# Performance work log

Measured on AMD Instinct MI355X. Metric: run time of the kernel, lower is better.

Reference implementation:

```python
import jax, jax.numpy as jnp
import numpy as np

HEADS = 4
RATES = (1, 2, 3, 4)
BN_EPS = 1e-5


def setup_inputs() -> dict:
    key = jax.random.key(0)
    k1, k2, k3 = jax.random.split(key, 3)
    b, c, h, w = 4, 256, 128, 128
    x = jax.random.normal(k1, (b, c, h, w), dtype=jnp.float32)
    w_qkv = jax.random.normal(k2, (3 * c, c), dtype=jnp.float32) * 0.02
    w_proj = jax.random.normal(k3, (c, c), dtype=jnp.float32) * 0.02
    gamma = jnp.ones((c,), dtype=jnp.float32)
    beta = jnp.zeros((c,), dtype=jnp.float32)
    return {"x": x, "w_qkv": w_qkv, "w_proj": w_proj, "gamma": gamma, "beta": beta}


def _neighbors(t, r, h, w):
    # t: [b, d, h, w] -> [b, d, 9, h, w], 3x3 dilated window with zero padding
    # (row-major kernel-position order matches F.unfold's C x kh x kw layout).
    tp = jnp.pad(t, ((0, 0), (0, 0), (r, r), (r, r)))
    return jnp.stack(
        [tp[:, :, i * r:i * r + h, j * r:j * r + w] for i in range(3) for j in range(3)],
        axis=2,
    )


def reference(x, w_qkv, w_proj, gamma, beta):
    b, c, h, w = x.shape
    d = c // HEADS
    # 1x1 conv == channel matmul
    qkv = jnp.einsum('oc,bchw->bohw', w_qkv, x)
    q, k, v = jnp.split(qkv, 3, axis=1)
    q = q.reshape(b, HEADS, d, h, w)
    k = k.reshape(b, HEADS, d, h, w)
    v = v.reshape(b, HEADS, d, h, w)
    outs = []
    for hi, r in enumerate(RATES):
        qh = q[:, hi]                      # [b, d, h, w]
        k_n = _neighbors(k[:, hi], r, h, w)  # [b, d, 9, h, w]
        v_n = _neighbors(v[:, hi], r, h, w)  # [b, d, 9, h, w]
        scores = jnp.einsum('bdhw,bdnhw->bnhw', qh, k_n)  # [b, 9, h, w]
        attn = jax.nn.softmax(scores, axis=1)
        outs.append(jnp.einsum('bdnhw,bnhw->bdhw', v_n, attn))
    y = jnp.concatenate(outs, axis=1)      # [b, c, h, w]
    y = jnp.einsum('oc,bchw->bohw', w_proj, y)
    # BatchNorm2d (training-mode batch statistics, biased variance)
    mean = y.mean(axis=(0, 2, 3), keepdims=True)
    var = ((y - mean) ** 2).mean(axis=(0, 2, 3), keepdims=True)
    yn = (y - mean) * jax.lax.rsqrt(var + BN_EPS)
    yn = yn * gamma[None, :, None, None] + beta[None, :, None, None]
    return x + jax.nn.silu(yn)
```

## Files before the change

### kernel.cpp

```cpp
#include <hip/hip_runtime.h>
#include <hip/hip_bf16.h>

#define BATCH 4
#define CCH   256
#define HH    128
#define WW    128
#define HWSZ  (HH * WW)
#define NHEADS 4
#define DHEAD 64
#define KDIM  256
#define PDIM  16384

typedef unsigned short u16;
typedef short bf16x8 __attribute__((ext_vector_type(8)));
typedef float f32x4  __attribute__((ext_vector_type(4)));

__device__ __forceinline__ float bf2f(u16 u) {
    return __uint_as_float(((unsigned)u) << 16);
}
__device__ __forceinline__ u16 f2bf(float f) {
    unsigned u = __float_as_uint(f);
    unsigned r = (u + 0x7fffu + ((u >> 16) & 1u)) >> 16;
    return (u16)r;
}
__device__ __forceinline__ unsigned pack2(float a, float b) {
    return (unsigned)f2bf(a) | ((unsigned)f2bf(b) << 16);
}
__device__ __forceinline__ void gl_lds16(const u16* g, u16* l) {
    __builtin_amdgcn_global_load_lds(
        (const __attribute__((address_space(1))) void*)g,
        (__attribute__((address_space(3))) void*)l, 16, 0, 0);
}

__global__ __launch_bounds__(256) void wconv(
    const float* __restrict__ wq, const float* __restrict__ wp,
    u16* __restrict__ wqb, u16* __restrict__ wpb)
{
    const int i = (blockIdx.x * 256 + threadIdx.x) * 4;
    const float4 v = (i < 196608)
        ? *reinterpret_cast<const float4*>(&wq[i])
        : *reinterpret_cast<const float4*>(&wp[i - 196608]);
    ushort4 o;
    o.x = f2bf(v.x); o.y = f2bf(v.y); o.z = f2bf(v.z); o.w = f2bf(v.w);
    if (i < 196608) *reinterpret_cast<ushort4*>(&wqb[i]) = o;
    else            *reinterpret_cast<ushort4*>(&wpb[i - 196608]) = o;
}

__global__ __launch_bounds__(256) void transpose_x(
    const float* __restrict__ x, u16* __restrict__ XT)
{
    __shared__ float t[32][33];
    const int b  = blockIdx.z;
    const int c0 = blockIdx.y * 32;
    const int p0 = blockIdx.x * 32;
    const int tid = threadIdx.x;

    #pragma unroll
    for (int it = 0; it < 4; ++it) {
        const int r = it * 8 + (tid >> 5);
        const int col = tid & 31;
        t[r][col] = x[((size_t)b * CCH + c0 + r) * HWSZ + p0 + col];
    }
    __syncthreads();
    #pragma unroll
    for (int it = 0; it < 2; ++it) {
        const int prow = it * 16 + (tid >> 4);
        const int cpair = (tid & 15) * 2;
        const float v0 = t[cpair][prow];
        const float v1 = t[cpair + 1][prow];
        ushort2 o; o.x = f2bf(v0); o.y = f2bf(v1);
        *reinterpret_cast<ushort2*>(
            &XT[((size_t)b * HWSZ + p0 + prow) * CCH + c0 + cpair]) = o;
    }
}

template <int OUT_MODE>
__global__ __launch_bounds__(256) void gemm_mfma(
    const u16* __restrict__ A, const u16* __restrict__ B,
    void* __restrict__ Y, long long b_zs,
    float* __restrict__ part, int batch0)
{
    constexpr int BK = 64;
    __shared__ u16 As[128 * BK];
    __shared__ u16 Bs[128 * BK];

    const int tid  = threadIdx.x;
    const int lane = tid & 63;
    const int w    = tid >> 6;
    const int wm   = w >> 1, wn = w & 1;
    const int o0   = blockIdx.y * 128;
    const int p0   = blockIdx.x * 128;
    const u16* Bz  = B + (size_t)blockIdx.z * b_zs;

    const int srow  = lane >> 3;
    const int sslot = (lane & 7) ^ srow;

    auto stage = [&](int c0) {
        #pragma unroll
        for (int j = 0; j < 4; ++j) {
            const int q = w * 4 + j;
            const int r = q * 8 + srow;
            gl_lds16(A  + (size_t)(o0 + r) * KDIM + c0 + sslot * 8, As + q * 512);
            gl_lds16(Bz + (size_t)(p0 + r) * KDIM + c0 + sslot * 8, Bs + q * 512);
        }
    };

    f32x4 acc[4][4];
    #pragma unroll
    for (int m = 0; m < 4; ++m)
        #pragma unroll
        for (int n = 0; n < 4; ++n)
            acc[m][n] = (f32x4){0.f, 0.f, 0.f, 0.f};

    stage(0);
    #pragma unroll
    for (int kt = 0; kt < KDIM / BK; ++kt) {
        __syncthreads();
        #pragma unroll
        for (int h = 0; h < 2; ++h) {
            bf16x8 af[4], bfr[4];
            #pragma unroll
            for (int m = 0; m < 4; ++m) {
                const int r  = wm * 64 + m * 16 + (lane & 15);
                const int sl = ((h << 2) | (lane >> 4)) ^ (r & 7);
                af[m] = *reinterpret_cast<const bf16x8*>(As + r * BK + sl * 8);
            }
            #pragma unroll
            for (int n = 0; n < 4; ++n) {
                const int r  = wn * 64 + n * 16 + (lane & 15);
                const int sl = ((h << 2) | (lane >> 4)) ^ (r & 7);
                bfr[n] = *reinterpret_cast<const bf16x8*>(Bs + r * BK + sl * 8);
            }
            #pragma unroll
            for (int m = 0; m < 4; ++m)
                #pragma unroll
                for (int n = 0; n < 4; ++n)
                    acc[m][n] = __builtin_amdgcn_mfma_f32_16x16x32_bf16(
                        af[m], bfr[n], acc[m][n], 0, 0, 0);
        }
        if (kt + 1 < KDIM / BK) {
            __syncthreads();
            stage((kt + 1) * BK);
        }
    }

    const int g = lane >> 4, ln15 = lane & 15;
    if (OUT_MODE == 1) {
        const int batch = batch0 + blockIdx.z;
        u16* Yz = (u16*)Y + (size_t)batch * CCH * HWSZ;
        float s[4][4], q2[4][4];
        #pragma unroll
        for (int m = 0; m < 4; ++m) {
            const int ow = o0 + wm * 64 + m * 16 + g * 4;
            #pragma unroll
            for (int j = 0; j < 4; ++j) { s[m][j] = 0.f; q2[m][j] = 0.f; }
            #pragma unroll
            for (int n = 0; n < 4; ++n) {
                const int pc = p0 + wn * 64 + n * 16 + ln15;
                #pragma unroll
                for (int j = 0; j < 4; ++j) {
                    const float v = acc[m][n][j];
                    Yz[(size_t)(ow + j) * PDIM + pc] = f2bf(v);
                    s[m][j]  += v;
                    q2[m][j] += v * v;
                }
            }
        }
        #pragma unroll
        for (int mask = 1; mask <= 8; mask <<= 1) {
            #pragma unroll
            for (int m = 0; m < 4; ++m)
                #pragma unroll
                for (int j = 0; j < 4; ++j) {
                    s[m][j]  += __shfl_xor(s[m][j],  mask);
                    q2[m][j] += __shfl_xor(q2[m][j], mask);
                }
        }
        if (ln15 == 0) {
            const int pxblk = batch * 256 + blockIdx.x * 2 + wn;
            #pragma unroll
            for (int m = 0; m < 4; ++m) {
                const int ow = o0 + wm * 64 + m * 16 + g * 4;
                #pragma unroll
                for (int j = 0; j < 4; ++j) {
                    const size_t idx = ((size_t)(ow + j) * 1024 + pxblk) * 2;
                    part[idx]     = s[m][j];
                    part[idx + 1] = q2[m][j];
                }
            }
        }
    } else {
        u16* Yz = (u16*)Y;
        const int z = blockIdx.z;
        #pragma unroll
        for (int m = 0; m < 4; ++m) {
            const int ow   = o0 + wm * 64 + m * 16 + g * 4;
            const int qkv  = ow >> 8;
            const int head = (ow >> 6) & 3;
            const int d    = ow & 63;
            u16* hbase = Yz + ((size_t)(z * NHEADS + head) * HWSZ) * 192
                            + qkv * 64 + d;
            #pragma unroll
            for (int n = 0; n < 4; ++n) {
                const int pc = p0 + wn * 64 + n * 16 + ln15;
                ushort4 st;
                st.x = f2bf(acc[m][n][0]);
                st.y = f2bf(acc[m][n][1]);
                st.z = f2bf(acc[m][n][2]);
                st.w = f2bf(acc[m][n][3]);
                *reinterpret_cast<ushort4*>(hbase + (size_t)pc * 192) = st;
            }
        }
    }
}

__global__ __launch_bounds__(256) void attn4(
    const u16* __restrict__ QKVH, u16* __restrict__ YT)
{
    const int hi  = blockIdx.y;
    const int tid = threadIdx.x;
    const int bxr = blockIdx.x;
    const int bx  = (bxr & 7) * 32 + (bxr >> 3);
    const int p   = bx * 64 + (tid >> 2);
    const int quarter = tid & 3;
    const int yy = p >> 7;
    const int xx = p & 127;
    const int r  = hi + 1;

    const u16* base = QKVH +
        ((size_t)(blockIdx.z * NHEADS + hi) * HWSZ) * 192;

    const uint4* qp = reinterpret_cast<const uint4*>(
        base + (size_t)p * 192 + quarter * 16);
    float qf[16];
    #pragma unroll
    for (int c4 = 0; c4 < 2; ++c4) {
        const uint4 t = qp[c4];
        const unsigned wv[4] = {t.x, t.y, t.z, t.w};
        #pragma unroll
        for (int d = 0; d < 4; ++d) {
            qf[c4 * 8 + d * 2 + 0] = __uint_as_float(wv[d] << 16);
            qf[c4 * 8 + d * 2 + 1] = __uint_as_float(wv[d] & 0xffff0000u);
        }
    }

    int   offs[9];
    float valid[9];
    #pragma unroll
    for (int n = 0; n < 9; ++n) {
        const int dy = (n / 3 - 1) * r;
        const int dx = (n % 3 - 1) * r;
        const int y2 = yy + dy, x2 = xx + dx;
        const bool ok = (y2 >= 0) && (y2 < HH) && (x2 >= 0) && (x2 < WW);
        valid[n] = ok ? 1.f : 0.f;
        const int y2c = min(max(y2, 0), HH - 1);
        const int x2c = min(max(x2, 0), WW - 1);
        offs[n] = y2c * WW + x2c;
    }

    float sc[9];
    #pragma unroll
    for (int n = 0; n < 9; ++n) {
        const uint4* kp = reinterpret_cast<const uint4*>(
            base + (size_t)offs[n] * 192 + 64 + quarter * 16);
        float s = 0.f;
        #pragma unroll
        for (int c4 = 0; c4 < 2; ++c4) {
            const uint4 t = kp[c4];
            const unsigned wv[4] = {t.x, t.y, t.z, t.w};
            #pragma unroll
            for (int d = 0; d < 4; ++d) {
                s += qf[c4 * 8 + d * 2 + 0] * __uint_as_float(wv[d] << 16);
                s += qf[c4 * 8 + d * 2 + 1] * __uint_as_float(wv[d] & 0xffff0000u);
            }
        }
        sc[n] = s;
    }
    #pragma unroll
    for (int n = 0; n < 9; ++n) {
        sc[n] += __shfl_xor(sc[n], 1);
        sc[n] += __shfl_xor(sc[n], 2);
        sc[n] *= valid[n];
    }

    float m = sc[0];
    #pragma unroll
    for (int n = 1; n < 9; ++n) m = fmaxf(m, sc[n]);
    float wgt[9], den = 0.f;
    #pragma unroll
    for (int n = 0; n < 9; ++n) { wgt[n] = __expf(sc[n] - m); den += wgt[n]; }
    const float inv = 1.f / den;
    #pragma unroll
    for (int n = 0; n < 9; ++n) wgt[n] *= inv * valid[n];

    float a[16];
    #pragma unroll
    for (int d = 0; d < 16; ++d) a[d] = 0.f;
    #pragma unroll
    for (int n = 0; n < 9; ++n) {
        const uint4* vp = reinterpret_cast<const uint4*>(
            base + (size_t)offs[n] * 192 + 128 + quarter * 16);
        const float wn_ = wgt[n];
        #pragma unroll
        for (int c4 = 0; c4 < 2; ++c4) {
            const uint4 t = vp[c4];
            const unsigned wv[4] = {t.x, t.y, t.z, t.w};
            #pragma unroll
            for (int d = 0; d < 4; ++d) {
                a[c4 * 8 + d * 2 + 0] += wn_ * __uint_as_float(wv[d] << 16);
                a[c4 * 8 + d * 2 + 1] += wn_ * __uint_as_float(wv[d] & 0xffff0000u);
            }
        }
    }

    u16* outp = YT + ((size_t)blockIdx.z * HWSZ + p) * CCH
                   + hi * DHEAD + quarter * 16;
    #pragma unroll
    for (int c4 = 0; c4 < 2; ++c4) {
        uint4 st;
        st.x = pack2(a[c4 * 8 + 0], a[c4 * 8 + 1]);
        st.y = pack2(a[c4 * 8 + 2], a[c4 * 8 + 3]);
        st.z = pack2(a[c4 * 8 + 4], a[c4 * 8 + 5]);
        st.w = pack2(a[c4 * 8 + 6], a[c4 * 8 + 7]);
        *reinterpret_cast<uint4*>(outp + c4 * 8) = st;
    }
}

__global__ __launch_bounds__(256) void bn_final(
    const float* __restrict__ part, float* __restrict__ stats)
{
    const int c = blockIdx.x;
    const int tid = threadIdx.x;
    float s = 0.f, q = 0.f;
    #pragma unroll
    for (int it = 0; it < 4; ++it) {
        const int i = tid + it * 256;
        s += part[((size_t)c * 1024 + i) * 2 + 0];
        q += part[((size_t)c * 1024 + i) * 2 + 1];
    }
    __shared__ float sh0[256], sh1[256];
    sh0[tid] = s; sh1[tid] = q;
    __syncthreads();
    for (int st = 128; st > 0; st >>= 1) {
        if (tid < st) { sh0[tid] += sh0[tid + st]; sh1[tid] += sh1[tid + st]; }
        __syncthreads();
    }
    if (tid == 0) {
        const float N = (float)(BATCH * HWSZ);
        const float mean = sh0[0] / N;
        const float var  = sh1[0] / N - mean * mean;
        stats[c]       = mean;
        stats[CCH + c] = rsqrtf(var + 1e-5f);
    }
}

__global__ __launch_bounds__(256) void bn_silu_res(
    const u16* __restrict__ yp, const float* __restrict__ x,
    const float* __restrict__ stats, const float* __restrict__ gamma,
    const float* __restrict__ beta, float* __restrict__ out)
{
    const size_t i = ((size_t)blockIdx.x * 256 + threadIdx.x) * 8;
    const int c = (int)((i >> 14) & 255);
    const float mean = stats[c];
    const float inv  = stats[CCH + c];
    const float g = gamma[c], bt = beta[c];

    const uint4 yv = *reinterpret_cast<const uint4*>(&yp[i]);
    const unsigned wv[4] = {yv.x, yv.y, yv.z, yv.w};
    float vo[8];
    #pragma unroll
    for (int d = 0; d < 4; ++d) {
        const float y0 = __uint_as_float(wv[d] << 16);
        const float y1 = __uint_as_float(wv[d] & 0xffff0000u);
        const float yn0 = (y0 - mean) * inv * g + bt;
        const float yn1 = (y1 - mean) * inv * g + bt;
        vo[d * 2 + 0] = yn0 / (1.f + __expf(-yn0));
        vo[d * 2 + 1] = yn1 / (1.f + __expf(-yn1));
    }
    const float4 x0 = *reinterpret_cast<const float4*>(&x[i]);
    const float4 x1 = *reinterpret_cast<const float4*>(&x[i + 4]);
    float4 o0, o1;
    o0.x = x0.x + vo[0]; o0.y = x0.y + vo[1];
    o0.z = x0.z + vo[2]; o0.w = x0.w + vo[3];
    o1.x = x1.x + vo[4]; o1.y = x1.y + vo[5];
    o1.z = x1.z + vo[6]; o1.w = x1.w + vo[7];
    *reinterpret_cast<float4*>(&out[i])     = o0;
    *reinterpret_cast<float4*>(&out[i + 4]) = o1;
}

extern "C" void kernel_launch(void* const* d_in, const int* in_sizes, int n_in,
                              void* d_out, int out_size, void* d_ws, size_t ws_size,
                              hipStream_t stream)
{
    const float* x      = (const float*)d_in[0];
    const float* w_qkv  = (const float*)d_in[1];
    const float* w_proj = (const float*)d_in[2];
    const float* gamma  = (const float*)d_in[3];
    const float* beta   = (const float*)d_in[4];
    float* out = (float*)d_out;

    u16*   XT    = (u16*)d_ws;
    u16*   YP    = XT;
    u16*   WQb   = XT + (size_t)BATCH * HWSZ * CCH;
    u16*   WPb   = WQb + 768 * CCH;
    float* part  = (float*)(WPb + CCH * CCH);
    float* stats = part + (size_t)CCH * 1024 * 2;
    u16*   QKVH2 = (u16*)(stats + 512);
    u16*   YT2   = QKVH2 + (size_t)2 * HWSZ * 768;

    wconv<<<256, 256, 0, stream>>>(w_qkv, w_proj, WQb, WPb);

    transpose_x<<<dim3(HWSZ / 32, CCH / 32, BATCH), 256, 0, stream>>>(x, XT);

    for (int pair = 0; pair < 2; ++pair) {
        const u16* Bx = XT + (size_t)pair * 2 * HWSZ * CCH;
        gemm_mfma<0><<<dim3(PDIM / 128, 768 / 128, 2), 256, 0, stream>>>(
            WQb, Bx, QKVH2, (long long)HWSZ * CCH, nullptr, 0);

        attn4<<<dim3(HWSZ / 64, NHEADS, 2), 256, 0, stream>>>(QKVH2, YT2);

        gemm_mfma<1><<<dim3(PDIM / 128, CCH / 128, 2), 256, 0, stream>>>(
            WPb, YT2, YP, (long long)HWSZ * CCH, part, pair * 2);
    }

    bn_final<<<CCH, 256, 0, stream>>>(part, stats);

    bn_silu_res<<<(unsigned)((size_t)BATCH * CCH * HWSZ / 8 / 256), 256, 0, stream>>>(
        YP, x, stats, gamma, beta, out);
}
```

Baseline: 162.8 us.

## Fuse attention with output projection GEMM and stage QKV epilogue through LDS

The attention kernel now computes all four heads for a 32-pixel tile, keeps the per-pixel 256-channel result in LDS, and runs the projection MFMA GEMM plus the BN partial statistics in the same kernel. This drops the YT intermediate round-trip and one launch per pair. The QKV GEMM epilogue now transposes its tile through LDS so it can write coalesced 16-byte rows into the head-major QKV layout. In exchange, each projection block reads W_proj straight from global memory with small 32-pixel tiles, the attention heads run serially inside one block, and the BN partial buffer doubles in size.

```diff
diff --git a/kernel.cpp b/kernel.cpp
--- a/kernel.cpp
+++ b/kernel.cpp
@@ -74,15 +74,15 @@
     }
 }
 
-template <int OUT_MODE>
-__global__ __launch_bounds__(256) void gemm_mfma(
+__global__ __launch_bounds__(256) void gemm_qkv(
     const u16* __restrict__ A, const u16* __restrict__ B,
-    void* __restrict__ Y, long long b_zs,
-    float* __restrict__ part, int batch0)
+    u16* __restrict__ QKVH, long long b_zs)
 {
     constexpr int BK = 64;
-    __shared__ u16 As[128 * BK];
-    __shared__ u16 Bs[128 * BK];
+    constexpr int CTP = 72;
+    __shared__ __align__(16) u16 lds[18432];
+    u16* As = lds;
+    u16* Bs = lds + 8192;
 
     const int tid  = threadIdx.x;
     const int lane = tid & 63;
@@ -90,7 +90,8 @@
     const int wm   = w >> 1, wn = w & 1;
     const int o0   = blockIdx.y * 128;
     const int p0   = blockIdx.x * 128;
-    const u16* Bz  = B + (size_t)blockIdx.z * b_zs;
+    const int z    = blockIdx.z;
+    const u16* Bz  = B + (size_t)z * b_zs;
 
     const int srow  = lane >> 3;
     const int sslot = (lane & 7) ^ srow;
@@ -144,185 +145,215 @@
         }
     }
 
+    __syncthreads();
+    u16* Ct = lds;
     const int g = lane >> 4, ln15 = lane & 15;
-    if (OUT_MODE == 1) {
-        const int batch = batch0 + blockIdx.z;
-        u16* Yz = (u16*)Y + (size_t)batch * CCH * HWSZ;
-        float s[4][4], q2[4][4];
+    #pragma unroll
+    for (int m = 0; m < 4; ++m) {
+        const int och = m * 16 + g * 4;
+        #pragma unroll
+        for (int n = 0; n < 4; ++n) {
+            const int px = wn * 64 + n * 16 + ln15;
+            uint2 w2;
+            w2.x = pack2(acc[m][n][0], acc[m][n][1]);
+            w2.y = pack2(acc[m][n][2], acc[m][n][3]);
+            *reinterpret_cast<uint2*>(&Ct[(wm * 128 + px) * CTP + och]) = w2;
+        }
+    }
+    __syncthreads();
+
+    const int c   = tid & 7;
+    const int sl  = (tid >> 3) & 1;
+    const int px0 = tid >> 4;
+    const int abs_slice = blockIdx.y * 2 + sl;
+    const int qkv  = abs_slice >> 2;
+    const int head = abs_slice & 3;
+    u16* dbase = QKVH + ((size_t)(z * NHEADS + head) * HWSZ) * 192 + qkv * 64 + c * 8;
+    #pragma unroll
+    for (int pass = 0; pass < 8; ++pass) {
+        const int px = px0 + pass * 16;
+        const uint4 val = *reinterpret_cast<const uint4*>(
+            &Ct[(sl * 128 + px) * CTP + c * 8]);
+        *reinterpret_cast<uint4*>(dbase + (size_t)(p0 + px) * 192) = val;
+    }
+}
+
+__global__ __launch_bounds__(256) void attn_proj(
+    const u16* __restrict__ QKVH, const u16* __restrict__ WP,
+    u16* __restrict__ YP, float* __restrict__ part, int batch0)
+{
+    __shared__ u16 y_lds[32][264];
+    const int tid = threadIdx.x;
+    const int z   = blockIdx.z;
+    const int batch = batch0 + z;
+    const int bxr = blockIdx.x;
+    const int bx  = (bxr & 7) * 64 + (bxr >> 3);
+    const int pxl = tid >> 3;
+    const int oct = tid & 7;
+    const int p   = bx * 32 + pxl;
+    const int yy = p >> 7, xx = p & 127;
+
+    #pragma unroll 1
+    for (int hi = 0; hi < NHEADS; ++hi) {
+        const int r = hi + 1;
+        const u16* base = QKVH + ((size_t)(z * NHEADS + hi) * HWSZ) * 192;
+
+        const uint4 qv = *reinterpret_cast<const uint4*>(
+            base + (size_t)p * 192 + oct * 8);
+        float qf[8];
+        {
+            const unsigned wv[4] = {qv.x, qv.y, qv.z, qv.w};
+            #pragma unroll
+            for (int d = 0; d < 4; ++d) {
+                qf[d * 2 + 0] = __uint_as_float(wv[d] << 16);
+                qf[d * 2 + 1] = __uint_as_float(wv[d] & 0xffff0000u);
+            }
+        }
+
+        int offs[9]; float valid[9];
+        #pragma unroll
+        for (int n = 0; n < 9; ++n) {
+            const int dy = (n / 3 - 1) * r;
+            const int dx = (n % 3 - 1) * r;
+            const int y2 = yy + dy, x2 = xx + dx;
+            const bool ok = (y2 >= 0) && (y2 < HH) && (x2 >= 0) && (x2 < WW);
+            valid[n] = ok ? 1.f : 0.f;
+            const int y2c = min(max(y2, 0), HH - 1);
+            const int x2c = min(max(x2, 0), WW - 1);
+            offs[n] = y2c * WW + x2c;
+        }
+
+        float sc[9];
+        #pragma unroll
+        for (int n = 0; n < 9; ++n) {
+            const uint4 kv = *reinterpret_cast<const uint4*>(
+                base + (size_t)offs[n] * 192 + 64 + oct * 8);
+            const unsigned wv[4] = {kv.x, kv.y, kv.z, kv.w};
+            float s = 0.f;
+            #pragma unroll
+            for (int d = 0; d < 4; ++d) {
+                s += qf[d * 2 + 0] * __uint_as_float(wv[d] << 16);
+                s += qf[d * 2 + 1] * __uint_as_float(wv[d] & 0xffff0000u);
+            }
+            sc[n] = s;
+        }
+        #pragma unroll
+        for (int n = 0; n < 9; ++n) {
+            sc[n] += __shfl_xor(sc[n], 1);
+            sc[n] += __shfl_xor(sc[n], 2);
+            sc[n] += __shfl_xor(sc[n], 4);
+            sc[n] *= valid[n];
+        }
+
+        float m = sc[0];
+        #pragma unroll
+        for (int n = 1; n < 9; ++n) m = fmaxf(m, sc[n]);
+        float wgt[9], den = 0.f;
+        #pragma unroll
+        for (int n = 0; n < 9; ++n) { wgt[n] = __expf(sc[n] - m); den += wgt[n]; }
+        const float inv = 1.f / den;
+        #pragma unroll
+        for (int n = 0; n < 9; ++n) wgt[n] *= inv * valid[n];
+
+        float a[8];
+        #pragma unroll
+        for (int d = 0; d < 8; ++d) a[d] = 0.f;
+        #pragma unroll
+        for (int n = 0; n < 9; ++n) {
+            const uint4 vv = *reinterpret_cast<const uint4*>(
+                base + (size_t)offs[n] * 192 + 128 + oct * 8);
+            const unsigned wv[4] = {vv.x, vv.y, vv.z, vv.w};
+            const float wn_ = wgt[n];
+            #pragma unroll
+            for (int d = 0; d < 4; ++d) {
+                a[d * 2 + 0] += wn_ * __uint_as_float(wv[d] << 16);
+                a[d * 2 + 1] += wn_ * __uint_as_float(wv[d] & 0xffff0000u);
+            }
+        }
+        uint4 st;
+        st.x = pack2(a[0], a[1]);
+        st.y = pack2(a[2], a[3]);
+        st.z = pack2(a[4], a[5]);
+        st.w = pack2(a[6], a[7]);
+        *reinterpret_cast<uint4*>(&y_lds[pxl][hi * 64 + oct * 8]) = st;
+    }
+    __syncthreads();
+
+    const int lane = tid & 63;
+    const int w    = tid >> 6;
+    const int ln15 = lane & 15, grp = lane >> 4;
+
+    f32x4 acc[4][2];
+    #pragma unroll
+    for (int m = 0; m < 4; ++m)
+        #pragma unroll
+        for (int n = 0; n < 2; ++n)
+            acc[m][n] = (f32x4){0.f, 0.f, 0.f, 0.f};
+
+    #pragma unroll
+    for (int ks = 0; ks < 8; ++ks) {
+        bf16x8 bfr[2];
+        #pragma unroll
+        for (int n = 0; n < 2; ++n) {
+            const int px = n * 16 + ln15;
+            bfr[n] = *reinterpret_cast<const bf16x8*>(
+                &y_lds[px][(ks * 4 + grp) * 8]);
+        }
+        bf16x8 af[4];
         #pragma unroll
         for (int m = 0; m < 4; ++m) {
-            const int ow = o0 + wm * 64 + m * 16 + g * 4;
-            #pragma unroll
-            for (int j = 0; j < 4; ++j) { s[m][j] = 0.f; q2[m][j] = 0.f; }
-            #pragma unroll
-            for (int n = 0; n < 4; ++n) {
-                const int pc = p0 + wn * 64 + n * 16 + ln15;
-                #pragma unroll
-                for (int j = 0; j < 4; ++j) {
-                    const float v = acc[m][n][j];
-                    Yz[(size_t)(ow + j) * PDIM + pc] = f2bf(v);
-                    s[m][j]  += v;
-                    q2[m][j] += v * v;
-                }
-            }
-        }
-        #pragma unroll
-        for (int mask = 1; mask <= 8; mask <<= 1) {
-            #pragma unroll
-            for (int m = 0; m < 4; ++m)
-                #pragma unroll
-                for (int j = 0; j < 4; ++j) {
-                    s[m][j]  += __shfl_xor(s[m][j],  mask);
-                    q2[m][j] += __shfl_xor(q2[m][j], mask);
-                }
-        }
-        if (ln15 == 0) {
-            const int pxblk = batch * 256 + blockIdx.x * 2 + wn;
-            #pragma unroll
-            for (int m = 0; m < 4; ++m) {
-                const int ow = o0 + wm * 64 + m * 16 + g * 4;
-                #pragma unroll
-                for (int j = 0; j < 4; ++j) {
-                    const size_t idx = ((size_t)(ow + j) * 1024 + pxblk) * 2;
-                    part[idx]     = s[m][j];
-                    part[idx + 1] = q2[m][j];
-                }
-            }
-        }
-    } else {
-        u16* Yz = (u16*)Y;
-        const int z = blockIdx.z;
+            const int row = w * 64 + m * 16 + ln15;
+            af[m] = *reinterpret_cast<const bf16x8*>(
+                WP + (size_t)row * 256 + ks * 32 + grp * 8);
+        }
+        #pragma unroll
+        for (int m = 0; m < 4; ++m)
+            #pragma unroll
+            for (int n = 0; n < 2; ++n)
+                acc[m][n] = __builtin_amdgcn_mfma_f32_16x16x32_bf16(
+                    af[m], bfr[n], acc[m][n], 0, 0, 0);
+    }
+
+    u16* Yz = YP + (size_t)batch * CCH * HWSZ;
+    float sums[4][4], sqs[4][4];
+    #pragma unroll
+    for (int m = 0; m < 4; ++m) {
+        const int row = w * 64 + m * 16 + grp * 4;
+        #pragma unroll
+        for (int j = 0; j < 4; ++j) {
+            const float v0 = acc[m][0][j], v1 = acc[m][1][j];
+            sums[m][j] = v0 + v1;
+            sqs[m][j]  = v0 * v0 + v1 * v1;
+        }
+        #pragma unroll
+        for (int n = 0; n < 2; ++n) {
+            const int pc = bx * 32 + n * 16 + ln15;
+            #pragma unroll
+            for (int j = 0; j < 4; ++j)
+                Yz[(size_t)(row + j) * PDIM + pc] = f2bf(acc[m][n][j]);
+        }
+    }
+    #pragma unroll
+    for (int mask = 1; mask <= 8; mask <<= 1)
+        #pragma unroll
+        for (int m = 0; m < 4; ++m)
+            #pragma unroll
+            for (int j = 0; j < 4; ++j) {
+                sums[m][j] += __shfl_xor(sums[m][j], mask);
+                sqs[m][j]  += __shfl_xor(sqs[m][j],  mask);
+            }
+    if (ln15 == 0) {
+        const int blk = batch * 512 + bx;
         #pragma unroll
         for (int m = 0; m < 4; ++m) {
-            const int ow   = o0 + wm * 64 + m * 16 + g * 4;
-            const int qkv  = ow >> 8;
-            const int head = (ow >> 6) & 3;
-            const int d    = ow & 63;
-            u16* hbase = Yz + ((size_t)(z * NHEADS + head) * HWSZ) * 192
-                            + qkv * 64 + d;
-            #pragma unroll
-            for (int n = 0; n < 4; ++n) {
-                const int pc = p0 + wn * 64 + n * 16 + ln15;
-                ushort4 st;
-                st.x = f2bf(acc[m][n][0]);
-                st.y = f2bf(acc[m][n][1]);
-                st.z = f2bf(acc[m][n][2]);
-                st.w = f2bf(acc[m][n][3]);
-                *reinterpret_cast<ushort4*>(hbase + (size_t)pc * 192) = st;
-            }
-        }
-    }
-}
-
-__global__ __launch_bounds__(256) void attn4(
-    const u16* __restrict__ QKVH, u16* __restrict__ YT)
-{
-    const int hi  = blockIdx.y;
-    const int tid = threadIdx.x;
-    const int bxr = blockIdx.x;
-    const int bx  = (bxr & 7) * 32 + (bxr >> 3);
-    const int p   = bx * 64 + (tid >> 2);
-    const int quarter = tid & 3;
-    const int yy = p >> 7;
-    const int xx = p & 127;
-    const int r  = hi + 1;
-
-    const u16* base = QKVH +
-        ((size_t)(blockIdx.z * NHEADS + hi) * HWSZ) * 192;
-
-    const uint4* qp = reinterpret_cast<const uint4*>(
-        base + (size_t)p * 192 + quarter * 16);
-    float qf[16];
-    #pragma unroll
-    for (int c4 = 0; c4 < 2; ++c4) {
-        const uint4 t = qp[c4];
-        const unsigned wv[4] = {t.x, t.y, t.z, t.w};
-        #pragma unroll
-        for (int d = 0; d < 4; ++d) {
-            qf[c4 * 8 + d * 2 + 0] = __uint_as_float(wv[d] << 16);
-            qf[c4 * 8 + d * 2 + 1] = __uint_as_float(wv[d] & 0xffff0000u);
-        }
-    }
-
-    int   offs[9];
-    float valid[9];
-    #pragma unroll
-    for (int n = 0; n < 9; ++n) {
-        const int dy = (n / 3 - 1) * r;
-        const int dx = (n % 3 - 1) * r;
-        const int y2 = yy + dy, x2 = xx + dx;
-        const bool ok = (y2 >= 0) && (y2 < HH) && (x2 >= 0) && (x2 < WW);
-        valid[n] = ok ? 1.f : 0.f;
-        const int y2c = min(max(y2, 0), HH - 1);
-        const int x2c = min(max(x2, 0), WW - 1);
-        offs[n] = y2c * WW + x2c;
-    }
-
-    float sc[9];
-    #pragma unroll
-    for (int n = 0; n < 9; ++n) {
-        const uint4* kp = reinterpret_cast<const uint4*>(
-            base + (size_t)offs[n] * 192 + 64 + quarter * 16);
-        float s = 0.f;
-        #pragma unroll
-        for (int c4 = 0; c4 < 2; ++c4) {
-            const uint4 t = kp[c4];
-            const unsigned wv[4] = {t.x, t.y, t.z, t.w};
-            #pragma unroll
-            for (int d = 0; d < 4; ++d) {
-                s += qf[c4 * 8 + d * 2 + 0] * __uint_as_float(wv[d] << 16);
-                s += qf[c4 * 8 + d * 2 + 1] * __uint_as_float(wv[d] & 0xffff0000u);
-            }
-        }
-        sc[n] = s;
-    }
-    #pragma unroll
-    for (int n = 0; n < 9; ++n) {
-        sc[n] += __shfl_xor(sc[n], 1);
-        sc[n] += __shfl_xor(sc[n], 2);
-        sc[n] *= valid[n];
-    }
-
-    float m = sc[0];
-    #pragma unroll
-    for (int n = 1; n < 9; ++n) m = fmaxf(m, sc[n]);
-    float wgt[9], den = 0.f;
-    #pragma unroll
-    for (int n = 0; n < 9; ++n) { wgt[n] = __expf(sc[n] - m); den += wgt[n]; }
-    const float inv = 1.f / den;
-    #pragma unroll
-    for (int n = 0; n < 9; ++n) wgt[n] *= inv * valid[n];
-
-    float a[16];
-    #pragma unroll
-    for (int d = 0; d < 16; ++d) a[d] = 0.f;
-    #pragma unroll
-    for (int n = 0; n < 9; ++n) {
-        const uint4* vp = reinterpret_cast<const uint4*>(
-            base + (size_t)offs[n] * 192 + 128 + quarter * 16);
-        const float wn_ = wgt[n];
-        #pragma unroll
-        for (int c4 = 0; c4 < 2; ++c4) {
-            const uint4 t = vp[c4];
-            const unsigned wv[4] = {t.x, t.y, t.z, t.w};
-            #pragma unroll
-            for (int d = 0; d < 4; ++d) {
-                a[c4 * 8 + d * 2 + 0] += wn_ * __uint_as_float(wv[d] << 16);
-                a[c4 * 8 + d * 2 + 1] += wn_ * __uint_as_float(wv[d] & 0xffff0000u);
-            }
-        }
-    }
-
-    u16* outp = YT + ((size_t)blockIdx.z * HWSZ + p) * CCH
-                   + hi * DHEAD + quarter * 16;
-    #pragma unroll
-    for (int c4 = 0; c4 < 2; ++c4) {
-        uint4 st;
-        st.x = pack2(a[c4 * 8 + 0], a[c4 * 8 + 1]);
-        st.y = pack2(a[c4 * 8 + 2], a[c4 * 8 + 3]);
-        st.z = pack2(a[c4 * 8 + 4], a[c4 * 8 + 5]);
-        st.w = pack2(a[c4 * 8 + 6], a[c4 * 8 + 7]);
-        *reinterpret_cast<uint4*>(outp + c4 * 8) = st;
+            const int row = w * 64 + m * 16 + grp * 4;
+            #pragma unroll
+            for (int j = 0; j < 4; ++j) {
+                const size_t idx = ((size_t)(row + j) * 2048 + blk) * 2;
+                part[idx]     = sums[m][j];
+                part[idx + 1] = sqs[m][j];
+            }
+        }
     }
 }
 
@@ -333,10 +364,10 @@
     const int tid = threadIdx.x;
     float s = 0.f, q = 0.f;
     #pragma unroll
-    for (int it = 0; it < 4; ++it) {
+    for (int it = 0; it < 8; ++it) {
         const int i = tid + it * 256;
-        s += part[((size_t)c * 1024 + i) * 2 + 0];
-        q += part[((size_t)c * 1024 + i) * 2 + 1];
+        s += part[((size_t)c * 2048 + i) * 2 + 0];
+        q += part[((size_t)c * 2048 + i) * 2 + 1];
     }
     __shared__ float sh0[256], sh1[256];
     sh0[tid] = s; sh1[tid] = q;
@@ -404,9 +435,8 @@
     u16*   WQb   = XT + (size_t)BATCH * HWSZ * CCH;
     u16*   WPb   = WQb + 768 * CCH;
     float* part  = (float*)(WPb + CCH * CCH);
-    float* stats = part + (size_t)CCH * 1024 * 2;
+    float* stats = part + (size_t)CCH * 2048 * 2;
     u16*   QKVH2 = (u16*)(stats + 512);
-    u16*   YT2   = QKVH2 + (size_t)2 * HWSZ * 768;
 
     wconv<<<256, 256, 0, stream>>>(w_qkv, w_proj, WQb, WPb);
 
@@ -414,13 +444,11 @@
 
     for (int pair = 0; pair < 2; ++pair) {
         const u16* Bx = XT + (size_t)pair * 2 * HWSZ * CCH;
-        gemm_mfma<0><<<dim3(PDIM / 128, 768 / 128, 2), 256, 0, stream>>>(
-            WQb, Bx, QKVH2, (long long)HWSZ * CCH, nullptr, 0);
-
-        attn4<<<dim3(HWSZ / 64, NHEADS, 2), 256, 0, stream>>>(QKVH2, YT2);
-
-        gemm_mfma<1><<<dim3(PDIM / 128, CCH / 128, 2), 256, 0, stream>>>(
-            WPb, YT2, YP, (long long)HWSZ * CCH, part, pair * 2);
+        gemm_qkv<<<dim3(PDIM / 128, 768 / 128, 2), 256, 0, stream>>>(
+            WQb, Bx, QKVH2, (long long)HWSZ * CCH);
+
+        attn_proj<<<dim3(HWSZ / 32, 1, 2), 256, 0, stream>>>(
+            QKVH2, WPb, YP, part, pair * 2);
     }
 
     bn_final<<<CCH, 256, 0, stream>>>(part, stats);
```

Result: no change. 163.3 us (+0.3%).
